# Kernel optimization log

Measured on AMD Instinct MI355X. Metric: run time of the kernel, lower is better.

## Reference

```python
import jax, jax.numpy as jnp
import numpy as np

D = 128      # embedding_dim
H = 8        # n_heads
L = 2        # n_encode_layers
FF = 512     # feed-forward hidden (4*D, AM default)
CLIP = 10.0  # tanh_clipping
EPS = 1e-5


def setup_inputs() -> dict:
    key = jax.random.key(0)
    ks = jax.random.split(key, 24)
    B, N = 32, 1000
    Nt = N + 2  # 2 depots + customers

    def w(k, shape, fan_in):
        return (jax.random.normal(k, shape, jnp.float32) / np.float32(np.sqrt(fan_in)))

    inp = {}
    inp["depot"] = jax.random.uniform(ks[0], (B, 2, 2), jnp.float32)
    inp["loc"] = jax.random.uniform(ks[1], (B, N, 2), jnp.float32)
    inp["demand"] = jax.random.uniform(ks[2], (B, N), jnp.float32)
    inp["mask"] = jax.random.randint(ks[3], (B, Nt), 0, 2) == 1
    # init embeddings
    inp["W_init_node"] = w(ks[4], (3, D), 3)
    inp["b_init_node"] = jnp.zeros((D,), jnp.float32)
    inp["W_init_depot"] = w(ks[5], (2, D), 2)
    inp["b_init_depot"] = jnp.zeros((D,), jnp.float32)
    # encoder layers (stacked over L)
    inp["enc_Wqkv"] = w(ks[6], (L, D, 3 * D), D)
    inp["enc_Wo"] = w(ks[7], (L, D, D), D)
    inp["enc_W1"] = w(ks[8], (L, D, FF), D)
    inp["enc_b1"] = jnp.zeros((L, FF), jnp.float32)
    inp["enc_W2"] = w(ks[9], (L, FF, D), FF)
    inp["enc_b2"] = jnp.zeros((L, D), jnp.float32)
    inp["bn1_s"] = jnp.ones((L, D), jnp.float32)
    inp["bn1_b"] = jnp.zeros((L, D), jnp.float32)
    inp["bn2_s"] = jnp.ones((L, D), jnp.float32)
    inp["bn2_b"] = jnp.zeros((L, D), jnp.float32)
    # decoder precompute / pointer attention
    inp["W_proj_node"] = w(ks[10], (D, 3 * D), D)   # project_node_embeddings_p2v
    inp["W_fixed_ctx"] = w(ks[11], (D, D), D)       # project_node_query_context
    inp["W_step_ctx"] = w(ks[12], (D, D), D)        # project_step_context_p2v
    inp["W_out"] = w(ks[13], (D, D), D)             # project_out_p2v
    return inp


def _bn(x, s, b):
    # BatchNorm1d over flattened (batch*nodes), training-mode stats, affine
    m = x.mean((0, 1))
    v = x.var((0, 1))
    return s * (x - m) * jax.lax.rsqrt(v + EPS) + b


def _mha(x, Wqkv, Wo):
    B, N, _ = x.shape
    dk = D // H
    q, k, v = jnp.split(x @ Wqkv, 3, axis=-1)

    def heads(t):
        return t.reshape(B, N, H, dk).transpose(0, 2, 1, 3)  # [B,H,N,dk]

    q, k, v = heads(q), heads(k), heads(v)
    attn = jax.nn.softmax(jnp.einsum('bhqd,bhkd->bhqk', q, k) / np.float32(np.sqrt(dk)), axis=-1)
    o = jnp.einsum('bhqk,bhkd->bhqd', attn, v).transpose(0, 2, 1, 3).reshape(B, N, D)
    return o @ Wo


def reference(depot, loc, demand, mask,
              W_init_node, b_init_node, W_init_depot, b_init_depot,
              enc_Wqkv, enc_Wo, enc_W1, enc_b1, enc_W2, enc_b2,
              bn1_s, bn1_b, bn2_s, bn2_b,
              W_proj_node, W_fixed_ctx, W_step_ctx, W_out):
    B = loc.shape[0]
    NEG = jnp.float32(-1e9)
    # --- init embeddings: depots via Linear(2,D), nodes via Linear(3,D) on (x,y,demand)
    depot_emb = depot @ W_init_depot + b_init_depot                      # [B,2,D]
    node_feat = jnp.concatenate([loc, demand[..., None]], -1)            # [B,N,3]
    node_emb = node_feat @ W_init_node + b_init_node                     # [B,N,D]
    h = jnp.concatenate([depot_emb, node_emb], 1)                        # [B,Nt,D]
    # --- graph encoder: L x (MHA + BN skip, FF + BN skip)
    for l in range(L):
        h = _bn(h + _mha(h, enc_Wqkv[l], enc_Wo[l]), bn1_s[l], bn1_b[l])
        ff = jax.nn.relu(h @ enc_W1[l] + enc_b1[l]) @ enc_W2[l] + enc_b2[l]
        h = _bn(h + ff, bn2_s[l], bn2_b[l])
    # --- fixed precompute (AttentionModelFixed)
    graph_embed = h.mean(1)                                              # [B,D]
    fixed_ctx = graph_embed @ W_fixed_ctx                                # [B,D]
    K_g, V_g, K_logit = jnp.split(h @ W_proj_node, 3, axis=-1)           # each [B,Nt,D]
    dk = D // H
    Kh = K_g.reshape(B, -1, H, dk).transpose(0, 2, 1, 3)                 # [B,H,Nt,dk]
    Vh = V_g.reshape(B, -1, H, dk).transpose(0, 2, 1, 3)
    # --- one glimpse+pointer step: context = fixed + projected first-depot step context
    query = fixed_ctx + h[:, 0, :] @ W_step_ctx                          # [B,D]
    qh = query.reshape(B, H, dk)                                         # [B,H,dk]
    compat = jnp.einsum('bhd,bhnd->bhn', qh, Kh) / np.float32(np.sqrt(dk))
    compat = jnp.where(mask[:, None, :], NEG, compat)                    # mask_inner
    attn = jax.nn.softmax(compat, axis=-1)
    glimpse = jnp.einsum('bhn,bhnd->bhd', attn, Vh).reshape(B, D) @ W_out
    logits = jnp.einsum('bd,bnd->bn', glimpse, K_logit) / np.float32(np.sqrt(D))
    logits = CLIP * jnp.tanh(logits)                                     # tanh clipping
    logits = jnp.where(mask, NEG, logits)                                # mask_logits
    log_p = jax.nn.log_softmax(logits, axis=-1)                          # [B,Nt]
    return log_p
```

## Files before the change

### kernel.cpp

```cpp
#include <hip/hip_runtime.h>

#define B_   32
#define NT_  1002
#define D_   128
#define H_   8
#define FF_  512
#define ROWS (B_ * NT_)
#define NEGV (-1e9f)
#define NTP  1024

typedef __bf16 bf16;
typedef __bf16 bf16x8 __attribute__((ext_vector_type(8)));
typedef __bf16 bf16x4 __attribute__((ext_vector_type(4)));
typedef float  f32x4  __attribute__((ext_vector_type(4)));
typedef float  f32x16 __attribute__((ext_vector_type(16)));

#if __has_builtin(__builtin_amdgcn_exp2f)
#define EXP2(x) __builtin_amdgcn_exp2f(x)
#else
#define EXP2(x) exp2f(x)
#endif

__device__ __forceinline__ int UNIT(int row, int seg) {
  return (row >> 4) * 64 + seg * 16 + (row & 15);
}

#define SZ_QKV (2*384*128)
#define SZ_WO  (2*128*128)
#define SZ_W1  (2*512*128)
#define SZ_W2  (2*128*512)
#define SZ_PROJ (384*128)

__global__ __launch_bounds__(256) void prep_w(
    const float* __restrict__ qkv, const float* __restrict__ wo, const float* __restrict__ w1,
    const float* __restrict__ w2, const float* __restrict__ proj, bf16* __restrict__ out) {
  int i = blockIdx.x * 256 + threadIdx.x;
  int j = i;
  float v;
  if (j < SZ_QKV) {
    int l = j / 49152, r = j % 49152; int n = r >> 7, k = r & 127;
    v = qkv[((size_t)l * 128 + k) * 384 + n];
  } else {
    j -= SZ_QKV;
    if (j < SZ_WO) {
      int l = j >> 14, r = j & 16383; int n = r >> 7, k = r & 127;
      v = wo[((size_t)l * 128 + k) * 128 + n];
    } else {
      j -= SZ_WO;
      if (j < SZ_W1) {
        int l = j >> 16, r = j & 65535; int n = r >> 7, k = r & 127;
        v = w1[((size_t)l * 128 + k) * 512 + n];
      } else {
        j -= SZ_W1;
        if (j < SZ_W2) {
          int l = j >> 16, r = j & 65535; int n = r >> 9, k = r & 511;
          v = w2[((size_t)l * 512 + k) * 128 + n];
        } else {
          j -= SZ_W2;
          int n = j >> 7, k = j & 127;
          v = proj[(size_t)k * 384 + n];
        }
      }
    }
  }
  out[i] = (bf16)v;
}

__global__ __launch_bounds__(256) void init_kernel(
    const float* __restrict__ depot, const float* __restrict__ loc, const float* __restrict__ demand,
    const float* __restrict__ Wn, const float* __restrict__ bn_, const float* __restrict__ Wd,
    const float* __restrict__ bd, bf16* __restrict__ hb) {
  int idx = blockIdx.x * 256 + threadIdx.x;
  if (idx >= ROWS * D_) return;
  int c = idx & 127;
  int row = idx >> 7;
  int b = row / NT_;
  int n = row - b * NT_;
  float v;
  if (n < 2) {
    const float* dp = depot + (b * 2 + n) * 2;
    v = dp[0] * Wd[c] + dp[1] * Wd[D_ + c] + bd[c];
  } else {
    int i = n - 2;
    const float* lp = loc + ((size_t)b * 1000 + i) * 2;
    v = lp[0] * Wn[c] + lp[1] * Wn[D_ + c] + demand[b * 1000 + i] * Wn[2 * D_ + c] + bn_[c];
  }
  hb[idx] = (bf16)v;
}

template<int N_, int K_, bool BIAS, bool RELU, bool RES, bool STATS>
__global__ __launch_bounds__(256) void mgemm(
    const bf16* __restrict__ A, const bf16* __restrict__ Wt,
    const float* __restrict__ bias, const bf16* __restrict__ R, bf16* __restrict__ Cout,
    float* __restrict__ ps, float* __restrict__ pq) {
  __shared__ bf16 AsF[2048];
  __shared__ bf16 BsF[4096];
  __shared__ float sredS[4][64];
  __shared__ float sredQ[4][64];
  int tid = threadIdx.x;
  int w = tid >> 6, l = tid & 63;
  int bm = blockIdx.y * 64, bn = blockIdx.x * 128;
  int wr = (w >> 1) * 32, wc = (w & 1) * 64;
  f32x4 acc[2][4] = {};
  int srow = tid >> 2, sseg = tid & 3;
  int uA = UNIT(srow, sseg);
  int uB0 = UNIT(srow, sseg), uB1 = UNIT(srow + 64, sseg);
  for (int k0 = 0; k0 < K_; k0 += 32) {
    __syncthreads();
    *(bf16x8*)&AsF[uA * 8] = *(const bf16x8*)&A[(size_t)(bm + srow) * K_ + k0 + sseg * 8];
    *(bf16x8*)&BsF[uB0 * 8] = *(const bf16x8*)&Wt[(size_t)(bn + srow) * K_ + k0 + sseg * 8];
    *(bf16x8*)&BsF[uB1 * 8] = *(const bf16x8*)&Wt[(size_t)(bn + srow + 64) * K_ + k0 + sseg * 8];
    __syncthreads();
    bf16x8 af[2], bfr[4];
#pragma unroll
    for (int mi = 0; mi < 2; ++mi)
      af[mi] = *(const bf16x8*)&AsF[(((wr >> 4) + mi) * 64 + (l >> 4) * 16 + (l & 15)) * 8];
#pragma unroll
    for (int ni = 0; ni < 4; ++ni)
      bfr[ni] = *(const bf16x8*)&BsF[(((wc >> 4) + ni) * 64 + (l >> 4) * 16 + (l & 15)) * 8];
#pragma unroll
    for (int mi = 0; mi < 2; ++mi)
#pragma unroll
      for (int ni = 0; ni < 4; ++ni)
        acc[mi][ni] = __builtin_amdgcn_mfma_f32_16x16x32_bf16(af[mi], bfr[ni], acc[mi][ni], 0, 0, 0);
  }
  float scol[4] = {}, qcol[4] = {};
#pragma unroll
  for (int mi = 0; mi < 2; ++mi)
#pragma unroll
    for (int ni = 0; ni < 4; ++ni)
#pragma unroll
      for (int r = 0; r < 4; ++r) {
        int row = bm + wr + mi * 16 + (l >> 4) * 4 + r;
        int col = bn + wc + ni * 16 + (l & 15);
        float v = acc[mi][ni][r];
        if (BIAS) v += bias[col];
        if (RELU) v = fmaxf(v, 0.f);
        if (RES)  v += (float)R[(size_t)row * N_ + col];
        if (STATS) { scol[ni] += v; qcol[ni] += v * v; }
        Cout[(size_t)row * N_ + col] = (bf16)v;
      }
  if (STATS) {
#pragma unroll
    for (int ni = 0; ni < 4; ++ni) {
      scol[ni] += __shfl_xor(scol[ni], 16); scol[ni] += __shfl_xor(scol[ni], 32);
      qcol[ni] += __shfl_xor(qcol[ni], 16); qcol[ni] += __shfl_xor(qcol[ni], 32);
    }
    __syncthreads();
    if (l < 16) {
#pragma unroll
      for (int ni = 0; ni < 4; ++ni) {
        sredS[w][ni * 16 + l] = scol[ni];
        sredQ[w][ni * 16 + l] = qcol[ni];
      }
    }
    __syncthreads();
    if (tid < 128) {
      int c = tid, cw = c >> 6, cc = c & 63;
      ps[(size_t)(bn + c) * 512 + blockIdx.y] = sredS[cw][cc] + sredS[cw + 2][cc];
      pq[(size_t)(bn + c) * 512 + blockIdx.y] = sredQ[cw][cc] + sredQ[cw + 2][cc];
    }
  }
}

__global__ __launch_bounds__(256) void mgemm_qkv(
    const bf16* __restrict__ A, const bf16* __restrict__ Wt,
    bf16* __restrict__ Qh, bf16* __restrict__ Kh, bf16* __restrict__ Vh) {
  __shared__ bf16 smem[128 * 68];
  bf16* AsF = smem;
  bf16* BsF = smem + 2048;
  bf16* Vt2 = smem;
  int tid = threadIdx.x;
  int w = tid >> 6, l = tid & 63;
  int bm = blockIdx.y * 64, bn = blockIdx.x * 128;
  int wr = (w >> 1) * 32, wc = (w & 1) * 64;
  f32x4 acc[2][4] = {};
  int srow = tid >> 2, sseg = tid & 3;
  int uA = UNIT(srow, sseg);
  int uB0 = UNIT(srow, sseg), uB1 = UNIT(srow + 64, sseg);
  for (int k0 = 0; k0 < 128; k0 += 32) {
    __syncthreads();
    *(bf16x8*)&AsF[uA * 8] = *(const bf16x8*)&A[(size_t)(bm + srow) * 128 + k0 + sseg * 8];
    *(bf16x8*)&BsF[uB0 * 8] = *(const bf16x8*)&Wt[(size_t)(bn + srow) * 128 + k0 + sseg * 8];
    *(bf16x8*)&BsF[uB1 * 8] = *(const bf16x8*)&Wt[(size_t)(bn + srow + 64) * 128 + k0 + sseg * 8];
    __syncthreads();
    bf16x8 af[2], bfr[4];
#pragma unroll
    for (int mi = 0; mi < 2; ++mi)
      af[mi] = *(const bf16x8*)&AsF[(((wr >> 4) + mi) * 64 + (l >> 4) * 16 + (l & 15)) * 8];
#pragma unroll
    for (int ni = 0; ni < 4; ++ni)
      bfr[ni] = *(const bf16x8*)&BsF[(((wc >> 4) + ni) * 64 + (l >> 4) * 16 + (l & 15)) * 8];
#pragma unroll
    for (int mi = 0; mi < 2; ++mi)
#pragma unroll
      for (int ni = 0; ni < 4; ++ni)
        acc[mi][ni] = __builtin_amdgcn_mfma_f32_16x16x32_bf16(af[mi], bfr[ni], acc[mi][ni], 0, 0, 0);
  }
  if (blockIdx.x < 2) {
    bf16* dst = (blockIdx.x == 0) ? Qh : Kh;
#pragma unroll
    for (int ni = 0; ni < 4; ++ni) {
      int cl = wc + ni * 16 + (l & 15);
      int hd = cl >> 4, c16 = cl & 15;
#pragma unroll
      for (int mi = 0; mi < 2; ++mi)
#pragma unroll
        for (int r = 0; r < 4; ++r) {
          int row = bm + wr + mi * 16 + (l >> 4) * 4 + r;
          int b = row / NT_;
          int n = row - b * NT_;
          dst[(((size_t)b * 8 + hd) * NTP + n) * 16 + c16] = (bf16)acc[mi][ni][r];
        }
    }
  } else {
    __syncthreads();
#pragma unroll
    for (int mi = 0; mi < 2; ++mi)
#pragma unroll
      for (int ni = 0; ni < 4; ++ni) {
        int cl = wc + ni * 16 + (l & 15);
        int r0 = wr + mi * 16 + (l >> 4) * 4;
        bf16x4 pk;
#pragma unroll
        for (int r = 0; r < 4; ++r) pk[r] = (bf16)acc[mi][ni][r];
        *(bf16x4*)&Vt2[cl * 68 + r0] = pk;
      }
    __syncthreads();
    int colg = tid >> 4, nl = tid & 15;
#pragma unroll
    for (int ci = 0; ci < 8; ++ci) {
      int lc = colg + ci * 16;
      int hd = lc >> 4, c16 = lc & 15;
#pragma unroll
      for (int ri = 0; ri < 4; ++ri) {
        int lrow = nl + ri * 16;
        int row = bm + lrow;
        int b = row / NT_;
        int n = row - b * NT_;
        Vh[(((size_t)b * 8 + hd) * 16 + c16) * NTP + n] = Vt2[lc * 68 + lrow];
      }
    }
  }
}

__global__ __launch_bounds__(256) void mattn(
    const bf16* __restrict__ Qh, const bf16* __restrict__ Kh,
    const bf16* __restrict__ Vh, bf16* __restrict__ ab) {
  __shared__ bf16 KsF[1024];
  __shared__ bf16 VtF[1024];
  __shared__ bf16 PsF[4][2048];
  int tid = threadIdx.x;
  int w = tid >> 6, l = tid & 63;
  int bh = blockIdx.x;
  int b = bh >> 3, hd = bh & 7;
  const bf16* Qp = Qh + (size_t)bh * NTP * 16;
  const bf16* Kp = Kh + (size_t)bh * NTP * 16;
  const bf16* Vp = Vh + (size_t)bh * 16 * NTP;
  int qbase = blockIdx.y * 128 + w * 32;
  int qrow = qbase + (l & 31); if (qrow >= NT_) qrow = NT_ - 1;
  bf16x8 qf = *(const bf16x8*)&Qp[qrow * 16 + (l >> 5) * 8];

  const float SC = 0.25f * 1.44269504088896f;
  const float MC = 8.0f * SC;
  f32x4 oacc[2] = {};
  f32x4 lacc[2] = {};
  bf16x8 ones;
#pragma unroll
  for (int i = 0; i < 8; ++i) ones[i] = (bf16)1.0f;
  const f32x16 zz = {0,0,0,0,0,0,0,0,0,0,0,0,0,0,0,0};

  for (int t = 0; t < 16; ++t) {
    int kb = t * 64;
    __syncthreads();
    if (tid < 128) {
      int key = (tid >> 6) * 32 + (tid & 31);
      int h2 = (tid >> 5) & 1;
      int krow = kb + key; if (krow >= NT_) krow = NT_ - 1;
      *(bf16x8*)&KsF[tid * 8] = *(const bf16x8*)&Kp[krow * 16 + h2 * 8];
    } else {
      int u = tid - 128;
      int seg = u >> 4, dim = u & 15;
      *(bf16x8*)&VtF[u * 8] = *(const bf16x8*)&Vp[dim * NTP + kb + seg * 8];
    }
    __syncthreads();

    f32x16 sv[2];
#pragma unroll
    for (int c = 0; c < 2; ++c) {
      bf16x8 kf = *(const bf16x8*)&KsF[(c * 64 + l) * 8];
      sv[c] = __builtin_amdgcn_mfma_f32_32x32x16_bf16(kf, qf, zz, 0, 0, 0);
    }
    if (kb + 64 > NT_) {
#pragma unroll
      for (int c = 0; c < 2; ++c)
#pragma unroll
        for (int r = 0; r < 16; ++r) {
          int key = kb + c * 32 + (r & 3) + 8 * (r >> 2) + 4 * (l >> 5);
          if (key >= NT_) sv[c][r] = -1e30f;
        }
    }
#pragma unroll
    for (int c = 0; c < 2; ++c)
#pragma unroll
      for (int r = 0; r < 16; ++r)
        sv[c][r] = EXP2(__builtin_fmaf(sv[c][r], SC, -MC));
    {
      int q = l & 31;
      int qh4 = q >> 4, ql = q & 15, half = (l >> 5) * 4;
#pragma unroll
      for (int c = 0; c < 2; ++c)
#pragma unroll
        for (int g2 = 0; g2 < 4; ++g2) {
          bf16x4 pk;
#pragma unroll
          for (int i = 0; i < 4; ++i) pk[i] = (bf16)sv[c][g2 * 4 + i];
          int unit = (c * 2 + qh4) * 64 + g2 * 16 + ql;
          *(bf16x4*)&PsF[w][unit * 8 + half] = pk;
        }
    }
#pragma unroll
    for (int kh = 0; kh < 2; ++kh) {
      bf16x8 vf = *(const bf16x8*)&VtF[(kh * 64 + l) * 8];
#pragma unroll
      for (int g = 0; g < 2; ++g) {
        bf16x8 pf = *(const bf16x8*)&PsF[w][((kh * 2 + g) * 64 + l) * 8];
        oacc[g] = __builtin_amdgcn_mfma_f32_16x16x32_bf16(pf, vf, oacc[g], 0, 0, 0);
        lacc[g] = __builtin_amdgcn_mfma_f32_16x16x32_bf16(pf, ones, lacc[g], 0, 0, 0);
      }
    }
  }
#pragma unroll
  for (int g = 0; g < 2; ++g)
#pragma unroll
    for (int r = 0; r < 4; ++r) {
      int qq = qbase + g * 16 + (l >> 4) * 4 + r;
      if (qq < NT_)
        ab[((size_t)b * NT_ + qq) * 128 + hd * 16 + (l & 15)] = (bf16)(oacc[g][r] / lacc[g][r]);
    }
}

__global__ __launch_bounds__(512) void stats_final(
    const float* __restrict__ ps, const float* __restrict__ pq,
    const float* __restrict__ sc, const float* __restrict__ bi, float* __restrict__ mi) {
  int tid = threadIdx.x;
  int c = tid >> 2, q4 = tid & 3;
  float s = 0.f, q = 0.f;
  for (int p = q4; p < 501; p += 4) { s += ps[c * 512 + p]; q += pq[c * 512 + p]; }
  s += __shfl_xor(s, 1); s += __shfl_xor(s, 2);
  q += __shfl_xor(q, 1); q += __shfl_xor(q, 2);
  if (q4 == 0) {
    float mean = s * (1.f / (float)ROWS);
    float var = q * (1.f / (float)ROWS) - mean * mean;
    float s2 = sc[c] * rsqrtf(var + 1e-5f);
    mi[c] = s2;
    mi[128 + c] = bi[c] - mean * s2;
  }
}

__global__ __launch_bounds__(256) void bn_apply(const bf16* __restrict__ X, const float* __restrict__ mi,
                                                bf16* __restrict__ Y) {
  __shared__ float sS[128], sB[128];
  if (threadIdx.x < 128) { sS[threadIdx.x] = mi[threadIdx.x]; sB[threadIdx.x] = mi[128 + threadIdx.x]; }
  __syncthreads();
  int chunk = blockIdx.x * 256 + threadIdx.x;
  if (chunk < ROWS * 16) {
    int c0 = (chunk & 15) * 8;
    bf16x8 x = *(const bf16x8*)&X[(size_t)chunk * 8];
    bf16x8 y;
#pragma unroll
    for (int i = 0; i < 8; ++i) y[i] = (bf16)__builtin_fmaf((float)x[i], sS[c0 + i], sB[c0 + i]);
    *(bf16x8*)&Y[(size_t)chunk * 8] = y;
  }
}

__global__ void ge_partial(const bf16* __restrict__ hb, float* __restrict__ part) {
  int b = blockIdx.x, ch = blockIdx.y, d = threadIdx.x;
  int n0 = ch * 126, n1 = n0 + 126; if (n1 > NT_) n1 = NT_;
  float s = 0.f;
  for (int n = n0; n < n1; ++n) s += (float)hb[((size_t)b * NT_ + n) * D_ + d];
  part[(b * 8 + ch) * D_ + d] = s;
}

__global__ void query_kernel(const float* __restrict__ part, const bf16* __restrict__ hb,
                             const float* __restrict__ Wf, const float* __restrict__ Ws,
                             float* __restrict__ qry) {
  __shared__ float sge[128], sh0[128];
  int b = blockIdx.x, d = threadIdx.x;
  float s = 0.f;
#pragma unroll
  for (int ch = 0; ch < 8; ++ch) s += part[(b * 8 + ch) * D_ + d];
  sge[d] = s * (1.f / (float)NT_);
  sh0[d] = (float)hb[(size_t)b * NT_ * D_ + d];
  __syncthreads();
  float q = 0.f;
  for (int k = 0; k < 128; ++k) q += sge[k] * Wf[k * D_ + d] + sh0[k] * Ws[k * D_ + d];
  qry[b * D_ + d] = q;
}

__global__ __launch_bounds__(256) void glimpse_kernel(
    const bf16* __restrict__ proj, const float* __restrict__ qry,
    const int* __restrict__ mask, float* __restrict__ glimpse) {
  int bid = blockIdx.x; int b = bid >> 3, hd = bid & 7;
  int tid = threadIdx.x;
  __shared__ float sq[16];
  __shared__ float sex[NT_];
  __shared__ float rmax[4];
  __shared__ float wacc[4][17];
  if (tid < 16) sq[tid] = qry[b * 128 + hd * 16 + tid];
  __syncthreads();
  const bf16* P = proj + (size_t)b * NT_ * 384;
  const int* Mk = mask + b * NT_;
  float lmax = -1e30f;
#pragma unroll
  for (int it = 0; it < 4; ++it) {
    int n = tid + it * 256;
    if (n < NT_) {
      float c = NEGV;
      if (!Mk[n]) {
        const bf16* kp = &P[(size_t)n * 384 + hd * 16];
        bf16x8 k0 = *(const bf16x8*)kp, k1 = *(const bf16x8*)(kp + 8);
        float d = 0.f;
#pragma unroll
        for (int i = 0; i < 8; ++i) d += sq[i] * (float)k0[i] + sq[8 + i] * (float)k1[i];
        c = d * 0.25f;
      }
      sex[n] = c;
      lmax = fmaxf(lmax, c);
    }
  }
#pragma unroll
  for (int o = 32; o > 0; o >>= 1) lmax = fmaxf(lmax, __shfl_xor(lmax, o));
  if ((tid & 63) == 0) rmax[tid >> 6] = lmax;
  __syncthreads();
  float mx = fmaxf(fmaxf(rmax[0], rmax[1]), fmaxf(rmax[2], rmax[3]));
  float acc[16];
#pragma unroll
  for (int i = 0; i < 16; ++i) acc[i] = 0.f;
  float lsum = 0.f;
#pragma unroll
  for (int it = 0; it < 4; ++it) {
    int n = tid + it * 256;
    if (n < NT_) {
      float e = __expf(sex[n] - mx);
      lsum += e;
      const bf16* vp = &P[(size_t)n * 384 + 128 + hd * 16];
      bf16x8 v0 = *(const bf16x8*)vp, v1 = *(const bf16x8*)(vp + 8);
#pragma unroll
      for (int i = 0; i < 8; ++i) { acc[i] += e * (float)v0[i]; acc[8 + i] += e * (float)v1[i]; }
    }
  }
#pragma unroll
  for (int o = 32; o > 0; o >>= 1) {
    lsum += __shfl_xor(lsum, o);
#pragma unroll
    for (int i = 0; i < 16; ++i) acc[i] += __shfl_xor(acc[i], o);
  }
  if ((tid & 63) == 0) {
    wacc[tid >> 6][16] = lsum;
#pragma unroll
    for (int i = 0; i < 16; ++i) wacc[tid >> 6][i] = acc[i];
  }
  __syncthreads();
  if (tid < 16) {
    float a = wacc[0][tid] + wacc[1][tid] + wacc[2][tid] + wacc[3][tid];
    float L = wacc[0][16] + wacc[1][16] + wacc[2][16] + wacc[3][16];
    glimpse[b * 128 + hd * 16 + tid] = a / L;
  }
}

__global__ void g2_kernel(const float* __restrict__ glimpse, const float* __restrict__ Wout,
                          float* __restrict__ g2) {
  __shared__ float sg[128];
  int b = blockIdx.x, d = threadIdx.x;
  sg[d] = glimpse[b * 128 + d];
  __syncthreads();
  float s = 0.f;
  for (int k = 0; k < 128; ++k) s += sg[k] * Wout[k * 128 + d];
  g2[b * 128 + d] = s;
}

__global__ __launch_bounds__(256) void logits_kernel(
    const bf16* __restrict__ proj, const float* __restrict__ g2,
    const int* __restrict__ mask, float* __restrict__ logits) {
  int b = blockIdx.y;
  int n = blockIdx.x * 256 + threadIdx.x;
  __shared__ float sg[128];
  if (threadIdx.x < 128) sg[threadIdx.x] = g2[b * 128 + threadIdx.x];
  __syncthreads();
  if (n >= NT_) return;
  const bf16* kp = &proj[((size_t)b * NT_ + n) * 384 + 256];
  float d = 0.f;
#pragma unroll
  for (int j = 0; j < 16; ++j) {
    bf16x8 v = *(const bf16x8*)&kp[j * 8];
#pragma unroll
    for (int i = 0; i < 8; ++i) d += sg[j * 8 + i] * (float)v[i];
  }
  d = 10.f * tanhf(d * 0.088388347648318447f);
  logits[b * NT_ + n] = mask[b * NT_ + n] ? NEGV : d;
}

__global__ __launch_bounds__(256) void lsm_kernel(const float* __restrict__ logits, float* __restrict__ out) {
  int b = blockIdx.x, tid = threadIdx.x;
  __shared__ float red[256];
  float mx = -1e30f;
  for (int n = tid; n < NT_; n += 256) mx = fmaxf(mx, logits[b * NT_ + n]);
  red[tid] = mx; __syncthreads();
  for (int s = 128; s > 0; s >>= 1) { if (tid < s) red[tid] = fmaxf(red[tid], red[tid + s]); __syncthreads(); }
  mx = red[0]; __syncthreads();
  float sm = 0.f;
  for (int n = tid; n < NT_; n += 256) sm += __expf(logits[b * NT_ + n] - mx);
  red[tid] = sm; __syncthreads();
  for (int s = 128; s > 0; s >>= 1) { if (tid < s) red[tid] += red[tid + s]; __syncthreads(); }
  float lse = mx + logf(red[0]);
  for (int n = tid; n < NT_; n += 256) out[(size_t)b * NT_ + n] = logits[b * NT_ + n] - lse;
}

extern "C" void kernel_launch(void* const* d_in, const int* in_sizes, int n_in,
                              void* d_out, int out_size, void* d_ws, size_t ws_size,
                              hipStream_t stream) {
  const float* depot        = (const float*)d_in[0];
  const float* loc          = (const float*)d_in[1];
  const float* demand       = (const float*)d_in[2];
  const int*   mask         = (const int*)d_in[3];
  const float* W_init_node  = (const float*)d_in[4];
  const float* b_init_node  = (const float*)d_in[5];
  const float* W_init_depot = (const float*)d_in[6];
  const float* b_init_depot = (const float*)d_in[7];
  const float* enc_Wqkv     = (const float*)d_in[8];
  const float* enc_Wo       = (const float*)d_in[9];
  const float* enc_W1       = (const float*)d_in[10];
  const float* enc_b1       = (const float*)d_in[11];
  const float* enc_W2       = (const float*)d_in[12];
  const float* enc_b2       = (const float*)d_in[13];
  const float* bn1_s        = (const float*)d_in[14];
  const float* bn1_b        = (const float*)d_in[15];
  const float* bn2_s        = (const float*)d_in[16];
  const float* bn2_b        = (const float*)d_in[17];
  const float* W_proj       = (const float*)d_in[18];
  const float* W_fixed      = (const float*)d_in[19];
  const float* W_step       = (const float*)d_in[20];
  const float* W_out        = (const float*)d_in[21];
  float* out = (float*)d_out;

  char* base = (char*)d_ws;
  bf16*  hb    = (bf16*)(base);
  bf16*  ab    = (bf16*)(base + 8208384);
  bf16*  Qh    = (bf16*)(base + 16416768);
  bf16*  Kh    = (bf16*)(base + 24805376);
  bf16*  Vh    = (bf16*)(base + 33193984);
  bf16*  xb    = Qh;
  bf16*  projb = Qh;
  bf16*  ff1b  = (bf16*)(base + 41582592);
  bf16*  wb    = (bf16*)(base + 74416128);
  float* ps    = (float*)(base + 75300864);
  float* pq    = (float*)(base + 75563008);
  float* mi    = (float*)(base + 75825152);
  float* qry   = (float*)(base + 75826176);
  float* glim  = (float*)(base + 75842560);
  float* g2    = (float*)(base + 75858944);
  float* gep   = ps;
  float* logit = pq;

  bf16* wt_qkv  = wb;
  bf16* wt_wo   = wb + SZ_QKV;
  bf16* wt_w1   = wb + SZ_QKV + SZ_WO;
  bf16* wt_w2   = wb + SZ_QKV + SZ_WO + SZ_W1;
  bf16* wt_proj = wb + SZ_QKV + SZ_WO + SZ_W1 + SZ_W2;

  prep_w<<<1728, 256, 0, stream>>>(enc_Wqkv, enc_Wo, enc_W1, enc_W2, W_proj, wb);
  init_kernel<<<(ROWS * D_ + 255) / 256, 256, 0, stream>>>(
      depot, loc, demand, W_init_node, b_init_node, W_init_depot, b_init_depot, hb);

  for (int l = 0; l < 2; ++l) {
    mgemm_qkv<<<dim3(3, 501), 256, 0, stream>>>(
        hb, wt_qkv + (size_t)l * 384 * 128, Qh, Kh, Vh);
    mattn<<<dim3(256, 8), 256, 0, stream>>>(Qh, Kh, Vh, ab);
    mgemm<128, 128, false, false, true, true><<<dim3(1, 501), 256, 0, stream>>>(
        ab, wt_wo + (size_t)l * 128 * 128, nullptr, hb, xb, ps, pq);
    stats_final<<<1, 512, 0, stream>>>(ps, pq, bn1_s + l * D_, bn1_b + l * D_, mi);
    bn_apply<<<2004, 256, 0, stream>>>(xb, mi, hb);
    mgemm<512, 128, true, true, false, false><<<dim3(4, 501), 256, 0, stream>>>(
        hb, wt_w1 + (size_t)l * 512 * 128, enc_b1 + (size_t)l * FF_, nullptr, ff1b, nullptr, nullptr);
    mgemm<128, 512, true, false, true, true><<<dim3(1, 501), 256, 0, stream>>>(
        ff1b, wt_w2 + (size_t)l * 128 * 512, enc_b2 + (size_t)l * D_, hb, xb, ps, pq);
    stats_final<<<1, 512, 0, stream>>>(ps, pq, bn2_s + l * D_, bn2_b + l * D_, mi);
    bn_apply<<<2004, 256, 0, stream>>>(xb, mi, hb);
  }

  mgemm<384, 128, false, false, false, false><<<dim3(3, 501), 256, 0, stream>>>(
      hb, wt_proj, nullptr, nullptr, projb, nullptr, nullptr);
  ge_partial<<<dim3(32, 8), 128, 0, stream>>>(hb, gep);
  query_kernel<<<32, 128, 0, stream>>>(gep, hb, W_fixed, W_step, qry);
  glimpse_kernel<<<256, 256, 0, stream>>>(projb, qry, mask, glim);
  g2_kernel<<<32, 128, 0, stream>>>(glim, W_out, g2);
  logits_kernel<<<dim3(4, 32), 256, 0, stream>>>(projb, g2, mask, logit);
  lsm_kernel<<<32, 256, 0, stream>>>(logit, out);
}
```

Before: 416.8 us.

## Fuse BatchNorm apply into GEMM consumers and fuse FFN into one kernel

```diff
diff --git a/kernel.cpp b/kernel.cpp
--- a/kernel.cpp
+++ b/kernel.cpp
@@ -21,8 +21,13 @@
 #define EXP2(x) exp2f(x)
 #endif
 
+#define MFMA16(a, b, c) __builtin_amdgcn_mfma_f32_16x16x32_bf16(a, b, c, 0, 0, 0)
+
 __device__ __forceinline__ int UNIT(int row, int seg) {
   return (row >> 4) * 64 + seg * 16 + (row & 15);
+}
+__device__ __forceinline__ int UNIT128(int row, int seg) {
+  return (row >> 4) * 256 + seg * 16 + (row & 15);
 }
 
 #define SZ_QKV (2*384*128)
@@ -88,11 +93,12 @@
   hb[idx] = (bf16)v;
 }
 
-template<int N_, int K_, bool BIAS, bool RELU, bool RES, bool STATS>
+template<int N_, int K_, bool BIAS, bool RELU, bool RES, bool STATS, bool BNA, bool BNR>
 __global__ __launch_bounds__(256) void mgemm(
     const bf16* __restrict__ A, const bf16* __restrict__ Wt,
     const float* __restrict__ bias, const bf16* __restrict__ R, bf16* __restrict__ Cout,
-    float* __restrict__ ps, float* __restrict__ pq) {
+    float* __restrict__ ps, float* __restrict__ pq,
+    const float* __restrict__ miA, const float* __restrict__ miR) {
   __shared__ bf16 AsF[2048];
   __shared__ bf16 BsF[4096];
   __shared__ float sredS[4][64];
@@ -103,13 +109,28 @@
   int wr = (w >> 1) * 32, wc = (w & 1) * 64;
   f32x4 acc[2][4] = {};
   int srow = tid >> 2, sseg = tid & 3;
-  int uA = UNIT(srow, sseg);
-  int uB0 = UNIT(srow, sseg), uB1 = UNIT(srow + 64, sseg);
+  int uA = UNIT(srow, sseg) * 8;
+  int uB0 = UNIT(srow, sseg) * 8, uB1 = UNIT(srow + 64, sseg) * 8;
   for (int k0 = 0; k0 < K_; k0 += 32) {
     __syncthreads();
-    *(bf16x8*)&AsF[uA * 8] = *(const bf16x8*)&A[(size_t)(bm + srow) * K_ + k0 + sseg * 8];
-    *(bf16x8*)&BsF[uB0 * 8] = *(const bf16x8*)&Wt[(size_t)(bn + srow) * K_ + k0 + sseg * 8];
-    *(bf16x8*)&BsF[uB1 * 8] = *(const bf16x8*)&Wt[(size_t)(bn + srow + 64) * K_ + k0 + sseg * 8];
+    {
+      bf16x8 x = *(const bf16x8*)&A[(size_t)(bm + srow) * K_ + k0 + sseg * 8];
+      if (BNA) {
+        int kc = k0 + sseg * 8;
+        f32x4 s0 = *(const f32x4*)&miA[kc],      s1 = *(const f32x4*)&miA[kc + 4];
+        f32x4 c0 = *(const f32x4*)&miA[128 + kc], c1 = *(const f32x4*)&miA[128 + kc + 4];
+        bf16x8 y;
+#pragma unroll
+        for (int i = 0; i < 4; ++i) y[i] = (bf16)__builtin_fmaf((float)x[i], s0[i], c0[i]);
+#pragma unroll
+        for (int i = 0; i < 4; ++i) y[4 + i] = (bf16)__builtin_fmaf((float)x[4 + i], s1[i], c1[i]);
+        *(bf16x8*)&AsF[uA] = y;
+      } else {
+        *(bf16x8*)&AsF[uA] = x;
+      }
+    }
+    *(bf16x8*)&BsF[uB0] = *(const bf16x8*)&Wt[(size_t)(bn + srow) * K_ + k0 + sseg * 8];
+    *(bf16x8*)&BsF[uB1] = *(const bf16x8*)&Wt[(size_t)(bn + srow + 64) * K_ + k0 + sseg * 8];
     __syncthreads();
     bf16x8 af[2], bfr[4];
 #pragma unroll
@@ -122,24 +143,30 @@
     for (int mi = 0; mi < 2; ++mi)
 #pragma unroll
       for (int ni = 0; ni < 4; ++ni)
-        acc[mi][ni] = __builtin_amdgcn_mfma_f32_16x16x32_bf16(af[mi], bfr[ni], acc[mi][ni], 0, 0, 0);
+        acc[mi][ni] = MFMA16(af[mi], bfr[ni], acc[mi][ni]);
   }
   float scol[4] = {}, qcol[4] = {};
 #pragma unroll
   for (int mi = 0; mi < 2; ++mi)
 #pragma unroll
-    for (int ni = 0; ni < 4; ++ni)
+    for (int ni = 0; ni < 4; ++ni) {
+      int col = bn + wc + ni * 16 + (l & 15);
+      float rs = 1.f, rb = 0.f;
+      if (RES && BNR) { rs = miR[col]; rb = miR[128 + col]; }
 #pragma unroll
       for (int r = 0; r < 4; ++r) {
         int row = bm + wr + mi * 16 + (l >> 4) * 4 + r;
-        int col = bn + wc + ni * 16 + (l & 15);
         float v = acc[mi][ni][r];
         if (BIAS) v += bias[col];
         if (RELU) v = fmaxf(v, 0.f);
-        if (RES)  v += (float)R[(size_t)row * N_ + col];
+        if (RES) {
+          float x = (float)R[(size_t)row * N_ + col];
+          v += BNR ? __builtin_fmaf(x, rs, rb) : x;
+        }
         if (STATS) { scol[ni] += v; qcol[ni] += v * v; }
         Cout[(size_t)row * N_ + col] = (bf16)v;
       }
+    }
   if (STATS) {
 #pragma unroll
     for (int ni = 0; ni < 4; ++ni) {
@@ -163,8 +190,9 @@
   }
 }
 
+template<bool BNA>
 __global__ __launch_bounds__(256) void mgemm_qkv(
-    const bf16* __restrict__ A, const bf16* __restrict__ Wt,
+    const bf16* __restrict__ A, const bf16* __restrict__ Wt, const float* __restrict__ miA,
     bf16* __restrict__ Qh, bf16* __restrict__ Kh, bf16* __restrict__ Vh) {
   __shared__ bf16 smem[128 * 68];
   bf16* AsF = smem;
@@ -176,13 +204,28 @@
   int wr = (w >> 1) * 32, wc = (w & 1) * 64;
   f32x4 acc[2][4] = {};
   int srow = tid >> 2, sseg = tid & 3;
-  int uA = UNIT(srow, sseg);
-  int uB0 = UNIT(srow, sseg), uB1 = UNIT(srow + 64, sseg);
+  int uA = UNIT(srow, sseg) * 8;
+  int uB0 = UNIT(srow, sseg) * 8, uB1 = UNIT(srow + 64, sseg) * 8;
   for (int k0 = 0; k0 < 128; k0 += 32) {
     __syncthreads();
-    *(bf16x8*)&AsF[uA * 8] = *(const bf16x8*)&A[(size_t)(bm + srow) * 128 + k0 + sseg * 8];
-    *(bf16x8*)&BsF[uB0 * 8] = *(const bf16x8*)&Wt[(size_t)(bn + srow) * 128 + k0 + sseg * 8];
-    *(bf16x8*)&BsF[uB1 * 8] = *(const bf16x8*)&Wt[(size_t)(bn + srow + 64) * 128 + k0 + sseg * 8];
+    {
+      bf16x8 x = *(const bf16x8*)&A[(size_t)(bm + srow) * 128 + k0 + sseg * 8];
+      if (BNA) {
+        int kc = k0 + sseg * 8;
+        f32x4 s0 = *(const f32x4*)&miA[kc],      s1 = *(const f32x4*)&miA[kc + 4];
+        f32x4 c0 = *(const f32x4*)&miA[128 + kc], c1 = *(const f32x4*)&miA[128 + kc + 4];
+        bf16x8 y;
+#pragma unroll
+        for (int i = 0; i < 4; ++i) y[i] = (bf16)__builtin_fmaf((float)x[i], s0[i], c0[i]);
+#pragma unroll
+        for (int i = 0; i < 4; ++i) y[4 + i] = (bf16)__builtin_fmaf((float)x[4 + i], s1[i], c1[i]);
+        *(bf16x8*)&AsF[uA] = y;
+      } else {
+        *(bf16x8*)&AsF[uA] = x;
+      }
+    }
+    *(bf16x8*)&BsF[uB0] = *(const bf16x8*)&Wt[(size_t)(bn + srow) * 128 + k0 + sseg * 8];
+    *(bf16x8*)&BsF[uB1] = *(const bf16x8*)&Wt[(size_t)(bn + srow + 64) * 128 + k0 + sseg * 8];
     __syncthreads();
     bf16x8 af[2], bfr[4];
 #pragma unroll
@@ -195,7 +238,7 @@
     for (int mi = 0; mi < 2; ++mi)
 #pragma unroll
       for (int ni = 0; ni < 4; ++ni)
-        acc[mi][ni] = __builtin_amdgcn_mfma_f32_16x16x32_bf16(af[mi], bfr[ni], acc[mi][ni], 0, 0, 0);
+        acc[mi][ni] = MFMA16(af[mi], bfr[ni], acc[mi][ni]);
   }
   if (blockIdx.x < 2) {
     bf16* dst = (blockIdx.x == 0) ? Qh : Kh;
@@ -241,6 +284,130 @@
         Vh[(((size_t)b * 8 + hd) * 16 + c16) * NTP + n] = Vt2[lc * 68 + lrow];
       }
     }
+  }
+}
+
+__global__ __launch_bounds__(256) void fffused(
+    const bf16* __restrict__ X, const float* __restrict__ mi,
+    const bf16* __restrict__ W1t, const float* __restrict__ bias1,
+    const bf16* __restrict__ W2t, const float* __restrict__ bias2,
+    bf16* __restrict__ Y, float* __restrict__ ps, float* __restrict__ pq) {
+  __shared__ bf16 A1[8192];
+  __shared__ bf16 A2[8192];
+  __shared__ bf16 BF[4096];
+  __shared__ float sredS[4][64];
+  __shared__ float sredQ[4][64];
+  int tid = threadIdx.x;
+  int w = tid >> 6, l = tid & 63;
+  int bm = blockIdx.x * 64;
+#pragma unroll
+  for (int it = 0; it < 4; ++it) {
+    int idx = it * 256 + tid;
+    int row = idx >> 4, seg = idx & 15;
+    bf16x8 x = *(const bf16x8*)&X[(size_t)(bm + row) * 128 + seg * 8];
+    f32x4 s0 = *(const f32x4*)&mi[seg * 8],       s1 = *(const f32x4*)&mi[seg * 8 + 4];
+    f32x4 c0 = *(const f32x4*)&mi[128 + seg * 8], c1 = *(const f32x4*)&mi[128 + seg * 8 + 4];
+    bf16x8 y;
+#pragma unroll
+    for (int i = 0; i < 4; ++i) y[i] = (bf16)__builtin_fmaf((float)x[i], s0[i], c0[i]);
+#pragma unroll
+    for (int i = 0; i < 4; ++i) y[4 + i] = (bf16)__builtin_fmaf((float)x[4 + i], s1[i], c1[i]);
+    *(bf16x8*)&A1[UNIT128(row, seg) * 8] = y;
+  }
+  int srow = tid >> 2, sseg = tid & 3;
+  int uB0 = UNIT(srow, sseg) * 8, uB1 = UNIT(srow + 64, sseg) * 8;
+  int wr = (w >> 1) * 32, wc = (w & 1) * 64;
+  f32x4 acc2[2][4] = {};
+
+  for (int nc = 0; nc < 4; ++nc) {
+    f32x4 acc1[2][4] = {};
+    for (int k0 = 0; k0 < 128; k0 += 32) {
+      __syncthreads();
+      *(bf16x8*)&BF[uB0] = *(const bf16x8*)&W1t[(size_t)(nc * 128 + srow) * 128 + k0 + sseg * 8];
+      *(bf16x8*)&BF[uB1] = *(const bf16x8*)&W1t[(size_t)(nc * 128 + srow + 64) * 128 + k0 + sseg * 8];
+      __syncthreads();
+      bf16x8 af[2], hf[4];
+#pragma unroll
+      for (int m2 = 0; m2 < 2; ++m2)
+        af[m2] = *(const bf16x8*)&BF[((w * 2 + m2) * 64 + (l >> 4) * 16 + (l & 15)) * 8];
+#pragma unroll
+      for (int ni = 0; ni < 4; ++ni)
+        hf[ni] = *(const bf16x8*)&A1[(ni * 256 + ((k0 >> 3) + (l >> 4)) * 16 + (l & 15)) * 8];
+#pragma unroll
+      for (int m2 = 0; m2 < 2; ++m2)
+#pragma unroll
+        for (int ni = 0; ni < 4; ++ni)
+          acc1[m2][ni] = MFMA16(af[m2], hf[ni], acc1[m2][ni]);
+    }
+#pragma unroll
+    for (int m2 = 0; m2 < 2; ++m2) {
+      int ffk0 = w * 32 + m2 * 16 + (l >> 4) * 4;
+      int seg = ffk0 >> 3, half = ffk0 & 7;
+#pragma unroll
+      for (int ni = 0; ni < 4; ++ni) {
+        bf16x4 pk;
+#pragma unroll
+        for (int r = 0; r < 4; ++r) {
+          float v = acc1[m2][ni][r] + bias1[nc * 128 + ffk0 + r];
+          pk[r] = (bf16)fmaxf(v, 0.f);
+        }
+        *(bf16x4*)&A2[(ni * 256 + seg * 16 + (l & 15)) * 8 + half] = pk;
+      }
+    }
+    __syncthreads();
+    for (int k0 = 0; k0 < 128; k0 += 32) {
+      if (k0) __syncthreads();
+      *(bf16x8*)&BF[uB0] = *(const bf16x8*)&W2t[(size_t)srow * 512 + nc * 128 + k0 + sseg * 8];
+      *(bf16x8*)&BF[uB1] = *(const bf16x8*)&W2t[(size_t)(srow + 64) * 512 + nc * 128 + k0 + sseg * 8];
+      __syncthreads();
+      bf16x8 a2f[2], b2f[4];
+#pragma unroll
+      for (int m2 = 0; m2 < 2; ++m2)
+        a2f[m2] = *(const bf16x8*)&A2[(((wr >> 4) + m2) * 256 + ((k0 >> 3) + (l >> 4)) * 16 + (l & 15)) * 8];
+#pragma unroll
+      for (int ni = 0; ni < 4; ++ni)
+        b2f[ni] = *(const bf16x8*)&BF[(((wc >> 4) + ni) * 64 + (l >> 4) * 16 + (l & 15)) * 8];
+#pragma unroll
+      for (int m2 = 0; m2 < 2; ++m2)
+#pragma unroll
+        for (int ni = 0; ni < 4; ++ni)
+          acc2[m2][ni] = MFMA16(a2f[m2], b2f[ni], acc2[m2][ni]);
+    }
+  }
+  float scol[4] = {}, qcol[4] = {};
+#pragma unroll
+  for (int m2 = 0; m2 < 2; ++m2)
+#pragma unroll
+    for (int ni = 0; ni < 4; ++ni) {
+      int col = wc + ni * 16 + (l & 15);
+      float bb = bias2[col];
+#pragma unroll
+      for (int r = 0; r < 4; ++r) {
+        int row = wr + m2 * 16 + (l >> 4) * 4 + r;
+        float res = (float)A1[UNIT128(row, col >> 3) * 8 + (col & 7)];
+        float v = acc2[m2][ni][r] + bb + res;
+        scol[ni] += v; qcol[ni] += v * v;
+        Y[(size_t)(bm + row) * 128 + col] = (bf16)v;
+      }
+    }
+#pragma unroll
+  for (int ni = 0; ni < 4; ++ni) {
+    scol[ni] += __shfl_xor(scol[ni], 16); scol[ni] += __shfl_xor(scol[ni], 32);
+    qcol[ni] += __shfl_xor(qcol[ni], 16); qcol[ni] += __shfl_xor(qcol[ni], 32);
+  }
+  __syncthreads();
+  if (l < 16) {
+#pragma unroll
+    for (int ni = 0; ni < 4; ++ni) {
+      sredS[w][ni * 16 + l] = scol[ni];
+      sredQ[w][ni * 16 + l] = qcol[ni];
+    }
+  }
+  __syncthreads();
+  if (tid < 128) {
+    int c = tid, cw = c >> 6, cc = c & 63;
+    ps[(size_t)c * 512 + blockIdx.x] = sredS[cw][cc] + sredS[cw + 2][cc];
+    pq[(size_t)c * 512 + blockIdx.x] = sredQ[cw][cc] + sredQ[cw + 2][cc];
   }
 }
 
@@ -325,8 +492,8 @@
 #pragma unroll
       for (int g = 0; g < 2; ++g) {
         bf16x8 pf = *(const bf16x8*)&PsF[w][((kh * 2 + g) * 64 + l) * 8];
-        oacc[g] = __builtin_amdgcn_mfma_f32_16x16x32_bf16(pf, vf, oacc[g], 0, 0, 0);
-        lacc[g] = __builtin_amdgcn_mfma_f32_16x16x32_bf16(pf, ones, lacc[g], 0, 0, 0);
+        oacc[g] = MFMA16(pf, vf, oacc[g]);
+        lacc[g] = MFMA16(pf, ones, lacc[g]);
       }
     }
   }
@@ -358,31 +525,19 @@
   }
 }
 
-__global__ __launch_bounds__(256) void bn_apply(const bf16* __restrict__ X, const float* __restrict__ mi,
-                                                bf16* __restrict__ Y) {
-  __shared__ float sS[128], sB[128];
-  if (threadIdx.x < 128) { sS[threadIdx.x] = mi[threadIdx.x]; sB[threadIdx.x] = mi[128 + threadIdx.x]; }
-  __syncthreads();
-  int chunk = blockIdx.x * 256 + threadIdx.x;
-  if (chunk < ROWS * 16) {
-    int c0 = (chunk & 15) * 8;
-    bf16x8 x = *(const bf16x8*)&X[(size_t)chunk * 8];
-    bf16x8 y;
-#pragma unroll
-    for (int i = 0; i < 8; ++i) y[i] = (bf16)__builtin_fmaf((float)x[i], sS[c0 + i], sB[c0 + i]);
-    *(bf16x8*)&Y[(size_t)chunk * 8] = y;
-  }
-}
-
-__global__ void ge_partial(const bf16* __restrict__ hb, float* __restrict__ part) {
+__global__ void ge_partial(const bf16* __restrict__ X, const float* __restrict__ mi,
+                           float* __restrict__ part) {
   int b = blockIdx.x, ch = blockIdx.y, d = threadIdx.x;
   int n0 = ch * 126, n1 = n0 + 126; if (n1 > NT_) n1 = NT_;
+  float sS = mi[d], sB = mi[128 + d];
   float s = 0.f;
-  for (int n = n0; n < n1; ++n) s += (float)hb[((size_t)b * NT_ + n) * D_ + d];
+  for (int n = n0; n < n1; ++n)
+    s += __builtin_fmaf((float)X[((size_t)b * NT_ + n) * D_ + d], sS, sB);
   part[(b * 8 + ch) * D_ + d] = s;
 }
 
-__global__ void query_kernel(const float* __restrict__ part, const bf16* __restrict__ hb,
+__global__ void query_kernel(const float* __restrict__ part, const bf16* __restrict__ X,
+                             const float* __restrict__ mi,
                              const float* __restrict__ Wf, const float* __restrict__ Ws,
                              float* __restrict__ qry) {
   __shared__ float sge[128], sh0[128];
@@ -391,7 +546,7 @@
 #pragma unroll
   for (int ch = 0; ch < 8; ++ch) s += part[(b * 8 + ch) * D_ + d];
   sge[d] = s * (1.f / (float)NT_);
-  sh0[d] = (float)hb[(size_t)b * NT_ * D_ + d];
+  sh0[d] = __builtin_fmaf((float)X[(size_t)b * NT_ * D_ + d], mi[d], mi[128 + d]);
   __syncthreads();
   float q = 0.f;
   for (int k = 0; k < 128; ++k) q += sge[k] * Wf[k * D_ + d] + sh0[k] * Ws[k * D_ + d];
@@ -545,21 +700,22 @@
   float* out = (float*)d_out;
 
   char* base = (char*)d_ws;
-  bf16*  hb    = (bf16*)(base);
+  bf16*  hb0   = (bf16*)(base);
   bf16*  ab    = (bf16*)(base + 8208384);
   bf16*  Qh    = (bf16*)(base + 16416768);
   bf16*  Kh    = (bf16*)(base + 24805376);
   bf16*  Vh    = (bf16*)(base + 33193984);
-  bf16*  xb    = Qh;
-  bf16*  projb = Qh;
-  bf16*  ff1b  = (bf16*)(base + 41582592);
+  bf16*  xb1   = Qh;
+  bf16*  xb2   = (bf16*)(base + 41582592);
+  bf16*  projb = (bf16*)(base + 49790976);
   bf16*  wb    = (bf16*)(base + 74416128);
   float* ps    = (float*)(base + 75300864);
   float* pq    = (float*)(base + 75563008);
-  float* mi    = (float*)(base + 75825152);
-  float* qry   = (float*)(base + 75826176);
-  float* glim  = (float*)(base + 75842560);
-  float* g2    = (float*)(base + 75858944);
+  float* mi1   = (float*)(base + 75825152);
+  float* mi2   = (float*)(base + 75826176);
+  float* qry   = (float*)(base + 75827200);
+  float* glim  = (float*)(base + 75843584);
+  float* g2    = (float*)(base + 75859968);
   float* gep   = ps;
   float* logit = pq;
 
@@ -571,28 +727,32 @@
 
   prep_w<<<1728, 256, 0, stream>>>(enc_Wqkv, enc_Wo, enc_W1, enc_W2, W_proj, wb);
   init_kernel<<<(ROWS * D_ + 255) / 256, 256, 0, stream>>>(
-      depot, loc, demand, W_init_node, b_init_node, W_init_depot, b_init_depot, hb);
+      depot, loc, demand, W_init_node, b_init_node, W_init_depot, b_init_depot, hb0);
 
   for (int l = 0; l < 2; ++l) {
-    mgemm_qkv<<<dim3(3, 501), 256, 0, stream>>>(
-        hb, wt_qkv + (size_t)l * 384 * 128, Qh, Kh, Vh);
+    const bf16* hin = (l == 0) ? hb0 : xb2;
+    if (l == 0)
+      mgemm_qkv<false><<<dim3(3, 501), 256, 0, stream>>>(hin, wt_qkv, nullptr, Qh, Kh, Vh);
+    else
+      mgemm_qkv<true><<<dim3(3, 501), 256, 0, stream>>>(hin, wt_qkv + (size_t)384 * 128, mi2, Qh, Kh, Vh);
     mattn<<<dim3(256, 8), 256, 0, stream>>>(Qh, Kh, Vh, ab);
-    mgemm<128, 128, false, false, true, true><<<dim3(1, 501), 256, 0, stream>>>(
-        ab, wt_wo + (size_t)l * 128 * 128, nullptr, hb, xb, ps, pq);
-    stats_final<<<1, 512, 0, stream>>>(ps, pq, bn1_s + l * D_, bn1_b + l * D_, mi);
-    bn_apply<<<2004, 256, 0, stream>>>(xb, mi, hb);
-    mgemm<512, 128, true, true, false, false><<<dim3(4, 501), 256, 0, stream>>>(
-        hb, wt_w1 + (size_t)l * 512 * 128, enc_b1 + (size_t)l * FF_, nullptr, ff1b, nullptr, nullptr);
-    mgemm<128, 512, true, false, true, true><<<dim3(1, 501), 256, 0, stream>>>(
-        ff1b, wt_w2 + (size_t)l * 128 * 512, enc_b2 + (size_t)l * D_, hb, xb, ps, pq);
-    stats_final<<<1, 512, 0, stream>>>(ps, pq, bn2_s + l * D_, bn2_b + l * D_, mi);
-    bn_apply<<<2004, 256, 0, stream>>>(xb, mi, hb);
-  }
-
-  mgemm<384, 128, false, false, false, false><<<dim3(3, 501), 256, 0, stream>>>(
-      hb, wt_proj, nullptr, nullptr, projb, nullptr, nullptr);
-  ge_partial<<<dim3(32, 8), 128, 0, stream>>>(hb, gep);
-  query_kernel<<<32, 128, 0, stream>>>(gep, hb, W_fixed, W_step, qry);
+    if (l == 0)
+      mgemm<128, 128, false, false, true, true, false, false><<<dim3(1, 501), 256, 0, stream>>>(
+          ab, wt_wo, nullptr, hin, xb1, ps, pq, nullptr, nullptr);
+    else
+      mgemm<128, 128, false, false, true, true, false, true><<<dim3(1, 501), 256, 0, stream>>>(
+          ab, wt_wo + (size_t)128 * 128, nullptr, hin, xb1, ps, pq, nullptr, mi2);
+    stats_final<<<1, 512, 0, stream>>>(ps, pq, bn1_s + l * D_, bn1_b + l * D_, mi1);
+    fffused<<<501, 256, 0, stream>>>(
+        xb1, mi1, wt_w1 + (size_t)l * 512 * 128, enc_b1 + (size_t)l * FF_,
+        wt_w2 + (size_t)l * 128 * 512, enc_b2 + (size_t)l * D_, xb2, ps, pq);
+    stats_final<<<1, 512, 0, stream>>>(ps, pq, bn2_s + l * D_, bn2_b + l * D_, mi2);
+  }
+
+  mgemm<384, 128, false, false, false, false, true, false><<<dim3(3, 501), 256, 0, stream>>>(
+      xb2, wt_proj, nullptr, nullptr, projb, nullptr, nullptr, mi2, nullptr);
+  ge_partial<<<dim3(32, 8), 128, 0, stream>>>(xb2, mi2, gep);
+  query_kernel<<<32, 128, 0, stream>>>(gep, xb2, mi2, W_fixed, W_step, qry);
   glimpse_kernel<<<256, 256, 0, stream>>>(projb, qry, mask, glim);
   g2_kernel<<<32, 128, 0, stream>>>(glim, W_out, g2);
   logits_kernel<<<dim3(4, 32), 256, 0, stream>>>(projb, g2, mask, logit);
```

Result: faster. 370.8 us (-11.1%).
